# Optimization experiments

Hardware: AMD Instinct MI355X
Metric: run time of the kernel (lower is better)

The kernel has to match this reference:

```python
import jax, jax.numpy as jnp
import numpy as np

MERSENNE_P = (1 << 31) - 1  # prime used by universal hashing


def _uhash_cols(random_numbers, n_full_cols, n_comp_cols):
    """Universal-hash map from full-weight column index -> compressed column index.
    h(j) = ((r0*j + r1) mod P) mod n_comp_cols  (ints stay well within int64).
    """
    j = jnp.arange(n_full_cols, dtype=jnp.int64)
    r0 = random_numbers[0]
    r1 = random_numbers[1]
    return ((r0 * j + r1) % MERSENNE_P) % n_comp_cols


def setup_inputs() -> dict:
    key = jax.random.key(0)
    k1, k2, k3 = jax.random.split(key, 3)
    in_features, out_features, redn_factor = 8192, 8192, 4
    init_scale = 1.0 / np.sqrt(in_features)
    x = jax.random.normal(k1, (64, in_features), dtype=jnp.float32)
    weight = jax.random.uniform(
        k2, (out_features, in_features // redn_factor), dtype=jnp.float32,
        minval=-init_scale, maxval=init_scale)
    random_numbers = jax.random.randint(k3, (4,), 1, 1048576, dtype=jnp.int64)
    return {"x": x, "weight": weight, "random_numbers": random_numbers,
            "redn_factor": 4}


def reference(x, weight, random_numbers, redn_factor):
    # x: [..., K]; weight (compressed): [N, K // redn_factor]
    orig_shape = x.shape
    K = orig_shape[-1]
    x2d = x.reshape(-1, K)                      # preprocess: flatten leading dims
    n_comp = weight.shape[1]
    col_idx = _uhash_cols(random_numbers, K, n_comp)   # [K] hashed gather indices
    w_full = weight[:, col_idx]                 # [N, K] expanded via hashed gather
    y = x2d @ w_full.T                          # [rows, N]
    return y.reshape(*orig_shape[:-1], y.shape[-1])  # postprocess
```

## Files before the change

### kernel.cpp

```cpp
#include <hip/hip_runtime.h>
#include <hip/hip_bf16.h>

#define K_FULL   8192
#define M_ROWS   64
#define N_OUT    8192
#define N_COMP   2048
#define P_MERS   2147483647


typedef __attribute__((ext_vector_type(8))) short bf16x8;
typedef __attribute__((ext_vector_type(4))) float f32x4;

__device__ __forceinline__ short f2bfs(float f) {
    __hip_bfloat16 h = __float2bfloat16(f);
    return *reinterpret_cast<short*>(&h);
}
__device__ __forceinline__ unsigned int pk2bf(float a, float b) {
    return (unsigned int)(unsigned short)f2bfs(a)
         | ((unsigned int)(unsigned short)f2bfs(b) << 16);
}

__device__ __forceinline__ int hash_col(int j, int rn0, int rn1, int rn2, int rn3) {
    if (rn1 == 0 && rn3 == 0) {
        unsigned long long xx = (unsigned long long)(unsigned int)rn0 * (unsigned int)j
                              + (unsigned long long)(unsigned int)rn2;
        unsigned long long t = (xx & (unsigned long long)P_MERS) + (xx >> 31);
        if (t >= (unsigned long long)P_MERS) t -= (unsigned long long)P_MERS;
        return (int)(t & (N_COMP - 1));
    } else {
        unsigned int t = (unsigned int)rn0 * (unsigned int)j + (unsigned int)rn1;
        int ti = (int)t;
        int m1 = ti % P_MERS;
        if (m1 < 0) m1 += P_MERS;
        return m1 & (N_COMP - 1);
    }
}

__global__ __launch_bounds__(1024) void k_xc(const float* __restrict__ x,
                                             const int* __restrict__ rn,
                                             unsigned int* __restrict__ xcF) {
    __shared__ float row[N_COMP];
    const int m = blockIdx.x;
    const int tid = threadIdx.x;
    row[tid] = 0.0f;
    row[tid + 1024] = 0.0f;
    const int rn0 = rn[0], rn1 = rn[1], rn2 = rn[2], rn3 = rn[3];
    __syncthreads();

    const float* xm = x + (size_t)m * K_FULL;
#pragma unroll
    for (int it = 0; it < 2; ++it) {
        int j0 = tid * 4 + it * 4096;
        float4 v = *(const float4*)(xm + j0);
        atomicAdd(&row[hash_col(j0 + 0, rn0, rn1, rn2, rn3)], v.x);
        atomicAdd(&row[hash_col(j0 + 1, rn0, rn1, rn2, rn3)], v.y);
        atomicAdd(&row[hash_col(j0 + 2, rn0, rn1, rn2, rn3)], v.z);
        atomicAdd(&row[hash_col(j0 + 3, rn0, rn1, rn2, rn3)], v.w);
    }
    __syncthreads();

    const int c0 = 2 * tid;
    const int s  = c0 >> 5;
    const int kg = (c0 >> 3) & 3;
    const int e0 = c0 & 7;
    const int g  = m >> 4;
    const int nr = m & 15;
    xcF[(((s * 4 + g) * 64 + kg * 16 + nr) << 2) + (e0 >> 1)] =
        pk2bf(row[c0], row[c0 + 1]);
}

__global__ __launch_bounds__(256) void k_gemm(const float* __restrict__ W,
                                              const unsigned short* __restrict__ xcF,
                                              float* __restrict__ y) {
    __shared__ float ys[4][M_ROWS][16];
    const int tid  = threadIdx.x;
    const int lane = tid & 63;
    const int w    = __builtin_amdgcn_readfirstlane(tid >> 6);
    const int nr   = lane & 15;
    const int kg   = lane >> 4;
    const int n0   = blockIdx.x * 16;
    const int rot  = blockIdx.x & 15;

    const float* wp = W + (size_t)(n0 + nr) * N_COMP + w * 512 + kg * 8;
    const unsigned short* ab = xcF + (size_t)w * 16 * 2048 + lane * 8;

    f32x4 acc0 = {0.f, 0.f, 0.f, 0.f};
    f32x4 acc1 = {0.f, 0.f, 0.f, 0.f};
    f32x4 acc2 = {0.f, 0.f, 0.f, 0.f};
    f32x4 acc3 = {0.f, 0.f, 0.f, 0.f};

#pragma unroll
    for (int s = 0; s < 16; ++s) {
        const int sk = (s + rot) & 15;
        float4 w0 = *(const float4*)(wp + sk * 32);
        float4 w1 = *(const float4*)(wp + sk * 32 + 4);
        const unsigned short* ap = ab + (size_t)sk * 2048;
        bf16x8 a0 = *(const bf16x8*)(ap);
        bf16x8 a1 = *(const bf16x8*)(ap + 512);
        bf16x8 a2 = *(const bf16x8*)(ap + 1024);
        bf16x8 a3 = *(const bf16x8*)(ap + 1536);
        bf16x8 b;
        b[0] = f2bfs(w0.x); b[1] = f2bfs(w0.y);
        b[2] = f2bfs(w0.z); b[3] = f2bfs(w0.w);
        b[4] = f2bfs(w1.x); b[5] = f2bfs(w1.y);
        b[6] = f2bfs(w1.z); b[7] = f2bfs(w1.w);
        acc0 = __builtin_amdgcn_mfma_f32_16x16x32_bf16(a0, b, acc0, 0, 0, 0);
        acc1 = __builtin_amdgcn_mfma_f32_16x16x32_bf16(a1, b, acc1, 0, 0, 0);
        acc2 = __builtin_amdgcn_mfma_f32_16x16x32_bf16(a2, b, acc2, 0, 0, 0);
        acc3 = __builtin_amdgcn_mfma_f32_16x16x32_bf16(a3, b, acc3, 0, 0, 0);
    }

#pragma unroll
    for (int j = 0; j < 4; ++j) {
        ys[w][ 0 + kg * 4 + j][nr] = acc0[j];
        ys[w][16 + kg * 4 + j][nr] = acc1[j];
        ys[w][32 + kg * 4 + j][nr] = acc2[j];
        ys[w][48 + kg * 4 + j][nr] = acc3[j];
    }
    __syncthreads();

#pragma unroll
    for (int i = 0; i < 4; ++i) {
        int o = tid + 256 * i;
        int m = o >> 4;
        int n = o & 15;
        float s = ys[0][m][n] + ys[1][m][n] + ys[2][m][n] + ys[3][m][n];
        y[(size_t)m * N_OUT + n0 + n] = s;
    }
}

extern "C" void kernel_launch(void* const* d_in, const int* in_sizes, int n_in,
                              void* d_out, int out_size, void* d_ws, size_t ws_size,
                              hipStream_t stream) {
    const float* x = (const float*)d_in[0];
    const float* W = (const float*)d_in[1];
    const int* rn  = (const int*)d_in[2];
    float* y       = (float*)d_out;

    unsigned int* xcF = (unsigned int*)d_ws;

    k_xc<<<M_ROWS, 1024, 0, stream>>>(x, rn, xcF);
    k_gemm<<<N_OUT / 16, 256, 0, stream>>>(W, (const unsigned short*)xcF, y);
}
```

Measured before the change: 31.24 us.

## Stage W tile through swizzled LDS with coalesced loads before MFMA loop

The GEMM kernel now loads each block's 16 weight rows with fully coalesced row-contiguous float4 reads, converts them to bf16, and stores them into a 64KB XOR-swizzled shared-memory tile. The MFMA loop then reads B operands from LDS instead of issuing strided per-lane global loads with a block rotation. This improves global access coalescing but adds a full barrier before compute, removes overlap of loads with MFMA, and uses 64KB of LDS per block, which limits occupancy.

```diff
diff --git a/kernel.cpp b/kernel.cpp
--- a/kernel.cpp
+++ b/kernel.cpp
@@ -72,44 +72,53 @@
 __global__ __launch_bounds__(256) void k_gemm(const float* __restrict__ W,
                                               const unsigned short* __restrict__ xcF,
                                               float* __restrict__ y) {
-    __shared__ float ys[4][M_ROWS][16];
+    __shared__ char smem[65536];
     const int tid  = threadIdx.x;
     const int lane = tid & 63;
     const int w    = __builtin_amdgcn_readfirstlane(tid >> 6);
     const int nr   = lane & 15;
     const int kg   = lane >> 4;
     const int n0   = blockIdx.x * 16;
-    const int rot  = blockIdx.x & 15;
 
-    const float* wp = W + (size_t)(n0 + nr) * N_COMP + w * 512 + kg * 8;
-    const unsigned short* ab = xcF + (size_t)w * 16 * 2048 + lane * 8;
+#pragma unroll
+    for (int i = 0; i < 4; ++i) {
+        const int r = (w * 4 + i);
+        const float* src = W + (size_t)(n0 + r) * N_COMP;
+        const int swz = (r & 7) << 4;
+        char* dst = smem + r * 4096;
+#pragma unroll
+        for (int q = 0; q < 8; ++q) {
+            float4 v = *(const float4*)(src + q * 256 + lane * 4);
+            uint2 p = { pk2bf(v.x, v.y), pk2bf(v.z, v.w) };
+            *(uint2*)(dst + ((q * 512 + lane * 8) ^ swz)) = p;
+        }
+    }
+    __syncthreads();
 
     f32x4 acc0 = {0.f, 0.f, 0.f, 0.f};
     f32x4 acc1 = {0.f, 0.f, 0.f, 0.f};
     f32x4 acc2 = {0.f, 0.f, 0.f, 0.f};
     f32x4 acc3 = {0.f, 0.f, 0.f, 0.f};
+    const unsigned short* ab = xcF + (size_t)w * 16 * 2048 + lane * 8;
+    const int bswz = (nr & 7) << 4;
 
 #pragma unroll
-    for (int s = 0; s < 16; ++s) {
-        const int sk = (s + rot) & 15;
-        float4 w0 = *(const float4*)(wp + sk * 32);
-        float4 w1 = *(const float4*)(wp + sk * 32 + 4);
+    for (int sk = 0; sk < 16; ++sk) {
+        bf16x8 b = *(const bf16x8*)(smem + nr * 4096
+                     + ((w * 1024 + sk * 64 + kg * 16) ^ bswz));
         const unsigned short* ap = ab + (size_t)sk * 2048;
         bf16x8 a0 = *(const bf16x8*)(ap);
         bf16x8 a1 = *(const bf16x8*)(ap + 512);
         bf16x8 a2 = *(const bf16x8*)(ap + 1024);
         bf16x8 a3 = *(const bf16x8*)(ap + 1536);
-        bf16x8 b;
-        b[0] = f2bfs(w0.x); b[1] = f2bfs(w0.y);
-        b[2] = f2bfs(w0.z); b[3] = f2bfs(w0.w);
-        b[4] = f2bfs(w1.x); b[5] = f2bfs(w1.y);
-        b[6] = f2bfs(w1.z); b[7] = f2bfs(w1.w);
         acc0 = __builtin_amdgcn_mfma_f32_16x16x32_bf16(a0, b, acc0, 0, 0, 0);
         acc1 = __builtin_amdgcn_mfma_f32_16x16x32_bf16(a1, b, acc1, 0, 0, 0);
         acc2 = __builtin_amdgcn_mfma_f32_16x16x32_bf16(a2, b, acc2, 0, 0, 0);
         acc3 = __builtin_amdgcn_mfma_f32_16x16x32_bf16(a3, b, acc3, 0, 0, 0);
     }
+    __syncthreads();
 
+    float (*ys)[M_ROWS][16] = (float (*)[M_ROWS][16])smem;
 #pragma unroll
     for (int j = 0; j < 4; ++j) {
         ys[w][ 0 + kg * 4 + j][nr] = acc0[j];
```

After: 34.81 us. 1.11x slower.
